# Performance work log

Measured on AMD Instinct MI355X. Metric: run time of the kernel, lower is better.

## Reference

```python
import jax, jax.numpy as jnp
import numpy as np

GRID = (32, 32)
LATENT = 256
ALPHA = 1.0
DECAY = 0.9


def _cdist(a, b):
    # Euclidean pairwise distance with a grad-safe sqrt (0 where d2==0, like torch.cdist).
    d2 = jnp.sum(a * a, -1)[:, None] + jnp.sum(b * b, -1)[None, :] - 2.0 * (a @ b.T)
    d2 = jnp.maximum(d2, 0.0)
    mask = d2 > 0
    return jnp.where(mask, jnp.sqrt(jnp.where(mask, d2, 1.0)), 0.0)


def setup_inputs() -> dict:
    key = jax.random.key(0)
    k1, k2 = jax.random.split(key)
    z = jax.random.normal(k1, (64, 512, 256), dtype=jnp.float32)
    nodes = jax.random.normal(k2, (GRID[0], GRID[1], LATENT), dtype=jnp.float32)
    return {"z": z, "nodes": nodes}


def reference(z, nodes):
    b, t, d = z.shape
    # time_decay^(seq_len - t - 1)
    tw = DECAY ** (t - 1 - jnp.arange(t, dtype=jnp.float32))
    z_flat = (z * tw[None, :, None]).reshape(b * t, d)   # (b t) d
    nodes_flat = nodes.reshape(-1, d)                     # n d

    dist = _cdist(z_flat, nodes_flat)                     # (b t) n
    q = 1.0 / (1.0 + dist / ALPHA) ** ((ALPHA + 1.0) / 2.0)
    q = q / jnp.sum(q, axis=-1, keepdims=True)            # L1 normalize rows
    q2 = q * q
    p = q2 / jnp.sum(q2, axis=0, keepdims=True)
    p = p / jnp.sum(p, axis=-1, keepdims=True)

    bmu = jnp.argmin(dist, axis=-1).reshape(b, t)         # int32

    # F.kl_div(q.log(), p, reduction='batchmean') = sum(p*(log p - log q)) / N
    kl_loss = jnp.sum(p * (jnp.log(p) - jnp.log(q))) / (b * t)
    diversity_loss = -jnp.mean(_cdist(nodes_flat, nodes_flat))
    time_smooth_loss = jnp.mean((z[:, 1:] - z[:, :-1]) ** 2) * DECAY

    # vectorized neighborhood consistency (python loop in the original is an
    # unweighted mean over all (b, t) adjacent pairs since seq_len is uniform)
    gw = GRID[1]
    pc = jnp.stack([bmu[:, :-1] // gw, bmu[:, :-1] % gw], axis=-1)
    nc = jnp.stack([bmu[:, 1:] // gw, bmu[:, 1:] % gw], axis=-1)
    neighbor_loss = jnp.mean(jnp.sum(jnp.abs(pc - nc), axis=-1).astype(jnp.float32))

    total_loss = kl_loss + 0.5 * diversity_loss + 0.3 * time_smooth_loss + 0.2 * neighbor_loss

    bmu_nodes = nodes_flat[bmu.reshape(-1)].reshape(b, t, d)
    som_z = z + 0.1 * (bmu_nodes - z)
    return (som_z, total_loss, kl_loss, diversity_loss, time_smooth_loss, neighbor_loss, q, bmu)
```

## Files before the change

kernel.cpp:

```cpp
#include <hip/hip_runtime.h>
#include <math.h>

#define Bb 64
#define Tt 512
#define Dd 256
#define Nn 1024
#define NROWS 32768

#define OUT_SOM 0L
#define OUT_SCAL 8388608L
#define OUT_Q 8388613L
#define OUT_BMU 41943045L

typedef __attribute__((ext_vector_type(8))) short bf16x8;
typedef __attribute__((ext_vector_type(4))) float f32x4;
typedef unsigned long long u64;

static __device__ __forceinline__ unsigned short f2bf(float x) {
  unsigned int u = __float_as_uint(x);
  unsigned int r = (u + 0x7fffu + ((u >> 16) & 1u)) >> 16;
  return (unsigned short)r;
}
static __device__ __forceinline__ float bf2f(unsigned short b) {
  return __uint_as_float(((unsigned int)b) << 16);
}

static __device__ __forceinline__ float block_reduce_sum(float v, float* sb) {
#pragma unroll
  for (int o = 32; o > 0; o >>= 1) v += __shfl_down(v, o, 64);
  const int lane = threadIdx.x & 63, w = threadIdx.x >> 6;
  if (lane == 0) sb[w] = v;
  __syncthreads();
  return (threadIdx.x == 0) ? (sb[0] + sb[1] + sb[2] + sb[3]) : 0.0f;
}

__global__ __launch_bounds__(256) void k_convz(const float* __restrict__ z,
                                               unsigned short* __restrict__ zhi,
                                               unsigned short* __restrict__ zlo,
                                               float* __restrict__ zn) {
  const int tid = threadIdx.x, lane = tid & 63, w = tid >> 6;
  const long row = (long)blockIdx.x * 4 + w;
  const int t = (int)(row & (Tt - 1));
  const float tw = powf(0.9f, (float)(Tt - 1 - t));
  const float4 v = ((const float4*)(z + row * Dd))[lane];
  float x[4] = {v.x * tw, v.y * tw, v.z * tw, v.w * tw};
  unsigned short h[4], l[4];
  float s = 0.f;
#pragma unroll
  for (int i = 0; i < 4; ++i) {
    h[i] = f2bf(x[i]);
    l[i] = f2bf(x[i] - bf2f(h[i]));
    s = fmaf(x[i], x[i], s);
  }
  *(ushort4*)(zhi + row * Dd + lane * 4) = make_ushort4(h[0], h[1], h[2], h[3]);
  *(ushort4*)(zlo + row * Dd + lane * 4) = make_ushort4(l[0], l[1], l[2], l[3]);
#pragma unroll
  for (int o = 32; o > 0; o >>= 1) s += __shfl_down(s, o, 64);
  if (lane == 0) zn[row] = s;
}

__global__ __launch_bounds__(256) void k_convn(const float* __restrict__ nodes,
                                               float* __restrict__ nt,
                                               float* __restrict__ nnorm,
                                               unsigned short* __restrict__ nhi,
                                               unsigned short* __restrict__ nlo) {
  __shared__ float sb[4];
  const int j = blockIdx.x, d = threadIdx.x;
  const float v = nodes[j * Dd + d];
  nt[(long)d * Nn + j] = v;
  const unsigned short h = f2bf(v);
  nhi[j * Dd + d] = h;
  nlo[j * Dd + d] = f2bf(v - bf2f(h));
  const float tot = block_reduce_sum(v * v, sb);
  if (threadIdx.x == 0) nnorm[j] = tot;
}

__global__ __launch_bounds__(256) void k_div(const float* __restrict__ nodes,
                                             const float* __restrict__ nt,
                                             const float* __restrict__ nnorm,
                                             float* __restrict__ scal) {
  __shared__ float ni[4][Dd];
  __shared__ float sb[4];
  const int tid = threadIdx.x;
  const int i0 = blockIdx.x * 4;
#pragma unroll
  for (int r = 0; r < 4; ++r) ni[r][tid] = nodes[(i0 + r) * Dd + tid];
  __syncthreads();
  float acc[4][4];
#pragma unroll
  for (int r = 0; r < 4; ++r)
#pragma unroll
    for (int jj = 0; jj < 4; ++jj) acc[r][jj] = 0.f;
  for (int d = 0; d < Dd; ++d) {
    float nj[4];
#pragma unroll
    for (int jj = 0; jj < 4; ++jj) nj[jj] = nt[(long)d * Nn + tid + 256 * jj];
#pragma unroll
    for (int r = 0; r < 4; ++r) {
      const float s = ni[r][d];
#pragma unroll
      for (int jj = 0; jj < 4; ++jj) acc[r][jj] = fmaf(s, nj[jj], acc[r][jj]);
    }
  }
  float sum = 0.f;
#pragma unroll
  for (int r = 0; r < 4; ++r) {
#pragma unroll
    for (int jj = 0; jj < 4; ++jj) {
      const float d2 = nnorm[i0 + r] + nnorm[tid + 256 * jj] - 2.f * acc[r][jj];
      sum += sqrtf(fmaxf(d2, 0.f));
    }
  }
  const float tot = block_reduce_sum(sum, sb);
  if (tid == 0) atomicAdd(&scal[1], tot);
}

__global__ __launch_bounds__(256, 2) void k_gemm(
    const unsigned short* __restrict__ zhi, const unsigned short* __restrict__ zlo,
    const unsigned short* __restrict__ nhi, const unsigned short* __restrict__ nlo,
    const float* __restrict__ zn, const float* __restrict__ nn,
    float* __restrict__ qout, float* __restrict__ part8,
    u64* __restrict__ bmup8) {
  __shared__ __align__(16) unsigned char smem[65536];

  const int tid = threadIdx.x, lane = tid & 63, wave = tid >> 6;
  const int wr = wave >> 1, wc = wave & 1;
  const int rl = lane & 15, kq = lane >> 4;
  const int bm = blockIdx.x & 255, bn = blockIdx.x >> 8;
  const long row0 = (long)bm * 128;
  const int col0 = bn * 128;

  auto stage = [&](int kt, int bufsel) {
    unsigned char* lb = smem + bufsel * 32768;
#pragma unroll
    for (int i = 0; i < 2; ++i) {
      const int rbase = (i * 4 + wave) * 16;
      const int r = rbase + (lane >> 2);
      const int kb = (lane & 3) ^ ((r >> 1) & 3);
      const long ea = (row0 + r) * Dd + kt * 32 + kb * 8;
      const long eb = (long)(col0 + r) * Dd + kt * 32 + kb * 8;
      const int lo = rbase * 64;
      __builtin_amdgcn_global_load_lds(
          (const __attribute__((address_space(1))) void*)(zhi + ea),
          (__attribute__((address_space(3))) void*)(lb + lo), 16, 0, 0);
      __builtin_amdgcn_global_load_lds(
          (const __attribute__((address_space(1))) void*)(zlo + ea),
          (__attribute__((address_space(3))) void*)(lb + 8192 + lo), 16, 0, 0);
      __builtin_amdgcn_global_load_lds(
          (const __attribute__((address_space(1))) void*)(nhi + eb),
          (__attribute__((address_space(3))) void*)(lb + 16384 + lo), 16, 0, 0);
      __builtin_amdgcn_global_load_lds(
          (const __attribute__((address_space(1))) void*)(nlo + eb),
          (__attribute__((address_space(3))) void*)(lb + 24576 + lo), 16, 0, 0);
    }
  };

  f32x4 acc[4][4];
#pragma unroll
  for (int i = 0; i < 4; ++i)
#pragma unroll
    for (int j = 0; j < 4; ++j) acc[i][j] = (f32x4){0.f, 0.f, 0.f, 0.f};

  stage(0, 0);
  __syncthreads();

  const int sx = (kq ^ ((rl >> 1) & 3)) << 4;

  for (int kt = 0; kt < 8; ++kt) {
    if (kt < 7) stage(kt + 1, (kt + 1) & 1);
    unsigned char* lb = smem + (kt & 1) * 32768;
    bf16x8 ah[4], al[4], bh[4], bl[4];
#pragma unroll
    for (int t = 0; t < 4; ++t) {
      const int ra = (wr * 64 + t * 16 + rl) * 64 + sx;
      ah[t] = *(const bf16x8*)(lb + ra);
      al[t] = *(const bf16x8*)(lb + 8192 + ra);
      const int rb = (wc * 64 + t * 16 + rl) * 64 + sx;
      bh[t] = *(const bf16x8*)(lb + 16384 + rb);
      bl[t] = *(const bf16x8*)(lb + 24576 + rb);
    }
#pragma unroll
    for (int i = 0; i < 4; ++i)
#pragma unroll
      for (int j = 0; j < 4; ++j) {
        acc[i][j] = __builtin_amdgcn_mfma_f32_16x16x32_bf16(ah[i], bh[j], acc[i][j], 0, 0, 0);
        acc[i][j] = __builtin_amdgcn_mfma_f32_16x16x32_bf16(ah[i], bl[j], acc[i][j], 0, 0, 0);
        acc[i][j] = __builtin_amdgcn_mfma_f32_16x16x32_bf16(al[i], bh[j], acc[i][j], 0, 0, 0);
      }
    __syncthreads();
  }

  float* srs = (float*)smem;
  u64* sbest = (u64*)(smem + 1024);
  float nnv[4];
#pragma unroll
  for (int j = 0; j < 4; ++j) nnv[j] = nn[col0 + wc * 64 + j * 16 + rl];

#pragma unroll
  for (int i = 0; i < 4; ++i) {
#pragma unroll
    for (int r = 0; r < 4; ++r) {
      const int lrow = wr * 64 + i * 16 + kq * 4 + r;
      const long grow = row0 + lrow;
      const float znv = zn[grow];
      float rs = 0.f;
      u64 best = ~0ull;
#pragma unroll
      for (int j = 0; j < 4; ++j) {
        const float dot = acc[i][j][r];
        const float d2 = znv + nnv[j] - 2.f * dot;
        const float dist = sqrtf(fmaxf(d2, 0.f));
        const float qr = 1.f / (1.f + dist);
        rs += qr;
        const int col = col0 + wc * 64 + j * 16 + rl;
        const u64 pk = ((u64)__float_as_uint(dist) << 32) | (unsigned int)col;
        best = pk < best ? pk : best;
        qout[grow * Nn + col] = qr;
      }
#pragma unroll
      for (int m = 1; m < 16; m <<= 1) {
        rs += __shfl_xor(rs, m, 64);
        const u64 o = __shfl_xor(best, m, 64);
        best = o < best ? o : best;
      }
      if (rl == 0) {
        srs[lrow * 2 + wc] = rs;
        sbest[lrow * 2 + wc] = best;
      }
    }
  }
  __syncthreads();
  if (tid < 128) {
    const long grow = row0 + tid;
    part8[grow * 8 + bn] = srs[tid * 2] + srs[tid * 2 + 1];
    const u64 a = sbest[tid * 2], b = sbest[tid * 2 + 1];
    bmup8[grow * 8 + bn] = a < b ? a : b;
  }
}

__global__ __launch_bounds__(256) void k_unpack(const u64* __restrict__ bmup8,
                                                float* __restrict__ bmuf) {
  const long row = (long)blockIdx.x * 256 + threadIdx.x;
  u64 best = ~0ull;
#pragma unroll
  for (int i = 0; i < 8; ++i) {
    const u64 v = bmup8[row * 8 + i];
    best = v < best ? v : best;
  }
  bmuf[row] = (float)(int)(unsigned int)(best & 0xffffffffull);
}

__global__ __launch_bounds__(256) void k_norm(float* __restrict__ q,
                                              const float* __restrict__ part8,
                                              float* __restrict__ colsum) {
  __shared__ float inv16[16];
  const int tid = threadIdx.x;
  const long r0 = (long)blockIdx.x * 16;
  if (tid < 16) {
    float s = 0.f;
    const float* p = part8 + (r0 + tid) * 8;
#pragma unroll
    for (int i = 0; i < 8; ++i) s += p[i];
    inv16[tid] = 1.f / s;
  }
  __syncthreads();
  float cs[4] = {0.f, 0.f, 0.f, 0.f};
  for (int r = 0; r < 16; ++r) {
    const long row = r0 + r;
    const float inv = inv16[r];
#pragma unroll
    for (int j = 0; j < 4; ++j) {
      const long idx = row * Nn + tid + 256 * j;
      const float v = q[idx] * inv;
      q[idx] = v;
      cs[j] = fmaf(v, v, cs[j]);
    }
  }
#pragma unroll
  for (int j = 0; j < 4; ++j) atomicAdd(&colsum[tid + 256 * j], cs[j]);
}

__global__ __launch_bounds__(256) void k_kl(const float* __restrict__ q,
                                            const float* __restrict__ colsum,
                                            float* __restrict__ scal) {
  __shared__ float csh[Nn];
  __shared__ float sb[4];
  const int tid = threadIdx.x, lane = tid & 63, wave = tid >> 6;
#pragma unroll
  for (int j = 0; j < 4; ++j) csh[tid + 256 * j] = colsum[tid + 256 * j];
  __syncthreads();
  const long r0 = (long)blockIdx.x * 16;
  float klp = 0.f;
  for (int rr = 0; rr < 4; ++rr) {
    const long row = r0 + rr * 4 + wave;
    float qv[16], u[16], s = 0.f;
#pragma unroll
    for (int j = 0; j < 16; ++j) {
      const int col = lane + 64 * j;
      const float t = q[row * Nn + col];
      qv[j] = t;
      const float uu = t * t / csh[col];
      u[j] = uu;
      s += uu;
    }
#pragma unroll
    for (int o = 1; o < 64; o <<= 1) s += __shfl_xor(s, o, 64);
    const float invS = 1.f / s;
#pragma unroll
    for (int j = 0; j < 16; ++j) {
      const float p = u[j] * invS;
      klp += p * (__logf(p) - __logf(qv[j]));
    }
  }
  const float tot = block_reduce_sum(klp, sb);
  if (tid == 0) atomicAdd(&scal[0], tot);
}

__global__ __launch_bounds__(256) void k_som(const float* __restrict__ z,
                                             const float* __restrict__ nodes,
                                             const float* __restrict__ bmuf,
                                             float* __restrict__ som,
                                             float* __restrict__ scal) {
  __shared__ float sb[4];
  const int tid = threadIdx.x;
  const long r0 = (long)blockIdx.x * 16;
  float ts = 0.f, zp = 0.f;
  if ((r0 & (Tt - 1)) > 0) zp = z[(r0 - 1) * Dd + tid];
  for (int r = 0; r < 16; ++r) {
    const long row = r0 + r;
    const float zc = z[row * Dd + tid];
    const int bi = (int)bmuf[row];
    const float nv = nodes[(long)bi * Dd + tid];
    som[row * Dd + tid] = zc + 0.1f * (nv - zc);
    if ((row & (Tt - 1)) > 0) {
      const float dd = zc - zp;
      ts = fmaf(dd, dd, ts);
    }
    zp = zc;
  }
  const float tot = block_reduce_sum(ts, sb);
  if (tid == 0) atomicAdd(&scal[2], tot);
}

__global__ __launch_bounds__(256) void k_nb(const float* __restrict__ bmuf,
                                            float* __restrict__ scal) {
  __shared__ float sb[4];
  const int idx = blockIdx.x * 256 + threadIdx.x;
  float s = 0.f;
  if (idx < Bb * (Tt - 1)) {
    const int b = idx / (Tt - 1);
    const int k = idx - b * (Tt - 1);
    const long row = (long)b * Tt + k;
    const int b1 = (int)bmuf[row], b2 = (int)bmuf[row + 1];
    s = (float)(abs((b1 >> 5) - (b2 >> 5)) + abs((b1 & 31) - (b2 & 31)));
  }
  const float tot = block_reduce_sum(s, sb);
  if (threadIdx.x == 0) atomicAdd(&scal[3], tot);
}

__global__ void k_final(const float* __restrict__ scal, float* __restrict__ o) {
  const float kl = scal[0] * (1.f / 32768.f);
  const float dv = -scal[1] * (1.f / (1024.f * 1024.f));
  const float ts = scal[2] * (0.9f / (64.f * 511.f * 256.f));
  const float nb = scal[3] * (1.f / 32704.f);
  o[0] = kl + 0.5f * dv + 0.3f * ts + 0.2f * nb;
  o[1] = kl;
  o[2] = dv;
  o[3] = ts;
  o[4] = nb;
}

__global__ __launch_bounds__(256) void k_prep_fb(const float* __restrict__ nodes,
                                                 float* __restrict__ nt,
                                                 float* __restrict__ nnorm) {
  __shared__ float sb[4];
  const int j = blockIdx.x, d = threadIdx.x;
  const float v = nodes[j * Dd + d];
  nt[(long)d * Nn + j] = v;
  const float tot = block_reduce_sum(v * v, sb);
  if (threadIdx.x == 0) nnorm[j] = tot;
}

__global__ __launch_bounds__(256) void k_dist_fb(
    const float* __restrict__ z, const float* __restrict__ nt,
    const float* __restrict__ nnorm, float* __restrict__ qout,
    float* __restrict__ srow, float* __restrict__ bmuf) {
  __shared__ float zt[Dd][65];
  __shared__ float rs4[4][64];
  __shared__ u64 cand[4][64];
  const int tid = threadIdx.x, lane = tid & 63, wave = tid >> 6;
  const long row0 = (long)blockIdx.x * 64;
  for (int k = 0; k < 64; ++k) {
    const int t = (int)((row0 + k) & (Tt - 1));
    const float tw = powf(0.9f, (float)(Tt - 1 - t));
    zt[tid][k] = z[(row0 + k) * Dd + tid] * tw;
  }
  __syncthreads();
  float zns = 0.f;
  for (int d = 0; d < Dd; ++d) {
    const float v = zt[d][lane];
    zns = fmaf(v, v, zns);
  }
  const long myrow = row0 + lane;
  float rsum = 0.f;
  u64 best = ~0ull;
  const int j0w = wave * 256;
  for (int chunk = 0; chunk < 16; ++chunk) {
    const int j0 = j0w + chunk * 16;
    float acc[16];
#pragma unroll
    for (int i = 0; i < 16; ++i) acc[i] = 0.f;
    const float* ntp = nt + j0;
    for (int d = 0; d < Dd; ++d) {
      const float zv = zt[d][lane];
      const float4 a = ((const float4*)ntp)[0];
      const float4 b = ((const float4*)ntp)[1];
      const float4 c = ((const float4*)ntp)[2];
      const float4 e = ((const float4*)ntp)[3];
      ntp += Nn;
      acc[0] = fmaf(zv, a.x, acc[0]); acc[1] = fmaf(zv, a.y, acc[1]);
      acc[2] = fmaf(zv, a.z, acc[2]); acc[3] = fmaf(zv, a.w, acc[3]);
      acc[4] = fmaf(zv, b.x, acc[4]); acc[5] = fmaf(zv, b.y, acc[5]);
      acc[6] = fmaf(zv, b.z, acc[6]); acc[7] = fmaf(zv, b.w, acc[7]);
      acc[8] = fmaf(zv, c.x, acc[8]); acc[9] = fmaf(zv, c.y, acc[9]);
      acc[10] = fmaf(zv, c.z, acc[10]); acc[11] = fmaf(zv, c.w, acc[11]);
      acc[12] = fmaf(zv, e.x, acc[12]); acc[13] = fmaf(zv, e.y, acc[13]);
      acc[14] = fmaf(zv, e.z, acc[14]); acc[15] = fmaf(zv, e.w, acc[15]);
    }
#pragma unroll
    for (int jj = 0; jj < 16; ++jj) {
      const int j = j0 + jj;
      const float d2 = zns + nnorm[j] - 2.f * acc[jj];
      const float dist = sqrtf(fmaxf(d2, 0.f));
      const float qr = 1.f / (1.f + dist);
      qout[myrow * Nn + j] = qr;
      rsum += qr;
      const u64 pk = ((u64)__float_as_uint(dist) << 32) | (unsigned int)j;
      best = pk < best ? pk : best;
    }
  }
  rs4[wave][lane] = rsum;
  cand[wave][lane] = best;
  __syncthreads();
  if (wave == 0) {
    const float s = rs4[0][lane] + rs4[1][lane] + rs4[2][lane] + rs4[3][lane];
    srow[myrow] = s;
    const u64 m0 = cand[0][lane] < cand[1][lane] ? cand[0][lane] : cand[1][lane];
    const u64 m1 = cand[2][lane] < cand[3][lane] ? cand[2][lane] : cand[3][lane];
    const u64 m = m0 < m1 ? m0 : m1;
    bmuf[myrow] = (float)(int)(unsigned int)(m & 0xffffffffull);
  }
}

__global__ __launch_bounds__(256) void k_norm_fb(float* __restrict__ q,
                                                 const float* __restrict__ srow,
                                                 float* __restrict__ colsum) {
  const int tid = threadIdx.x;
  const long r0 = (long)blockIdx.x * 16;
  float cs[4] = {0.f, 0.f, 0.f, 0.f};
  for (int r = 0; r < 16; ++r) {
    const long row = r0 + r;
    const float inv = 1.f / srow[row];
#pragma unroll
    for (int j = 0; j < 4; ++j) {
      const long idx = row * Nn + tid + 256 * j;
      const float v = q[idx] * inv;
      q[idx] = v;
      cs[j] = fmaf(v, v, cs[j]);
    }
  }
#pragma unroll
  for (int j = 0; j < 4; ++j) atomicAdd(&colsum[tid + 256 * j], cs[j]);
}

extern "C" void kernel_launch(void* const* d_in, const int* in_sizes, int n_in,
                              void* d_out, int out_size, void* d_ws, size_t ws_size,
                              hipStream_t stream) {
  const float* z = (const float*)d_in[0];
  const float* nodes = (const float*)d_in[1];
  float* out = (float*)d_out;
  unsigned char* ws = (unsigned char*)d_ws;

  float* som = out + OUT_SOM;
  float* scal_out = out + OUT_SCAL;
  float* qout = out + OUT_Q;
  float* bmuf = out + OUT_BMU;

  const size_t NEED = 37888016;
  if (ws_size >= NEED) {
    unsigned short* zhi = (unsigned short*)(ws + 0);
    unsigned short* zlo = (unsigned short*)(ws + 16777216);
    unsigned short* nhi = (unsigned short*)(ws + 33554432);
    unsigned short* nlo = (unsigned short*)(ws + 34078720);
    float* zn = (float*)(ws + 34603008);
    float* ntpart = (float*)(ws + 34734080);
    u64* bmup8 = (u64*)(ws + 35782656);
    float* nnorm = (float*)(ws + 37879808);
    float* colsum = (float*)(ws + 37883904);
    float* scal = (float*)(ws + 37888000);

    hipMemsetAsync(colsum, 0, 4096 + 16, stream);

    k_convz<<<8192, 256, 0, stream>>>(z, zhi, zlo, zn);
    k_convn<<<1024, 256, 0, stream>>>(nodes, ntpart, nnorm, nhi, nlo);
    k_div<<<256, 256, 0, stream>>>(nodes, ntpart, nnorm, scal);
    k_gemm<<<2048, 256, 0, stream>>>(zhi, zlo, nhi, nlo, zn, nnorm, qout, ntpart, bmup8);
    k_unpack<<<128, 256, 0, stream>>>(bmup8, bmuf);
    k_norm<<<2048, 256, 0, stream>>>(qout, ntpart, colsum);
    k_kl<<<2048, 256, 0, stream>>>(qout, colsum, scal);
    k_som<<<2048, 256, 0, stream>>>(z, nodes, bmuf, som, scal);
    k_nb<<<128, 256, 0, stream>>>(bmuf, scal);
    k_final<<<1, 1, 0, stream>>>(scal, scal_out);
  } else {
    float* wsf = (float*)ws;
    float* nt = wsf;
    float* nnorm = wsf + 262144;
    float* srow = wsf + 263168;
    float* colsum = wsf + 295936;
    float* scal = wsf + 296960;

    hipMemsetAsync(colsum, 0, (1024 + 4) * sizeof(float), stream);
    k_prep_fb<<<1024, 256, 0, stream>>>(nodes, nt, nnorm);
    k_div<<<256, 256, 0, stream>>>(nodes, nt, nnorm, scal);
    k_dist_fb<<<512, 256, 0, stream>>>(z, nt, nnorm, qout, srow, bmuf);
    k_norm_fb<<<2048, 256, 0, stream>>>(qout, srow, colsum);
    k_kl<<<2048, 256, 0, stream>>>(qout, colsum, scal);
    k_som<<<2048, 256, 0, stream>>>(z, nodes, bmuf, som, scal);
    k_nb<<<128, 256, 0, stream>>>(bmuf, scal);
    k_final<<<1, 1, 0, stream>>>(scal, scal_out);
  }
}
```

Measured before the change: 298.0 us.

## Fuse row normalization into GEMM, pre-swizzle MFMA operands, merge small kernels

The z and nodes conversion kernels are merged into one, and each writes bf16 hi/lo operands already arranged in MFMA fragment order. A new GEMM kernel processes 32 full rows per block across all 1024 columns, reading fragments straight from global memory without an LDS stage. Because whole rows stay in one block, it can finish the row-sum normalization, the BMU selection and the column-sum accumulation in place, which removes the separate unpack and normalize passes and their extra read/write of q. Other changes: the diversity loss moves to an MFMA kernel, the KL kernel is reworked algebraically to use one pass with precomputed reciprocal and log column sums, and the neighbor loss is folded into the som kernel. The cost is that GEMM operands are no longer reused through LDS, so global/L2 traffic for the node operands goes up.

```diff
diff --git a/kernel.cpp b/kernel.cpp
--- a/kernel.cpp
+++ b/kernel.cpp
@@ -15,6 +15,7 @@
 typedef __attribute__((ext_vector_type(8))) short bf16x8;
 typedef __attribute__((ext_vector_type(4))) float f32x4;
 typedef unsigned long long u64;
+typedef unsigned short ushortT;
 
 static __device__ __forceinline__ unsigned short f2bf(float x) {
   unsigned int u = __float_as_uint(x);
@@ -34,293 +35,312 @@
   return (threadIdx.x == 0) ? (sb[0] + sb[1] + sb[2] + sb[3]) : 0.0f;
 }
 
-__global__ __launch_bounds__(256) void k_convz(const float* __restrict__ z,
-                                               unsigned short* __restrict__ zhi,
-                                               unsigned short* __restrict__ zlo,
-                                               float* __restrict__ zn) {
+__global__ __launch_bounds__(256) void k_conv(
+    const float* __restrict__ z, const float* __restrict__ nodes,
+    ushortT* __restrict__ zhiF, ushortT* __restrict__ zloF, float* __restrict__ zn,
+    ushortT* __restrict__ nhiF, ushortT* __restrict__ nloF, float* __restrict__ nnorm) {
+  __shared__ float sm[32 * 260];
+  const int tid = threadIdx.x;
+  if (blockIdx.x < 1024) {
+    const int rt = blockIdx.x;
+    const long row0 = (long)rt * 32;
+    const int r = tid >> 3, c8 = tid & 7;
+    const long rowg = row0 + r;
+    const int t = (int)(rowg & (Tt - 1));
+    const float tw = powf(0.9f, (float)(Tt - 1 - t));
+    float nrm = 0.f;
+#pragma unroll
+    for (int k = 0; k < 8; ++k) {
+      const int c4 = c8 + k * 8;
+      float4 v = ((const float4*)(z + rowg * Dd))[c4];
+      v.x *= tw; v.y *= tw; v.z *= tw; v.w *= tw;
+      *(float4*)&sm[r * 260 + c4 * 4] = v;
+      nrm += v.x * v.x + v.y * v.y + v.z * v.z + v.w * v.w;
+    }
+    nrm += __shfl_xor(nrm, 1, 64);
+    nrm += __shfl_xor(nrm, 2, 64);
+    nrm += __shfl_xor(nrm, 4, 64);
+    if (c8 == 0) zn[rowg] = nrm;
+    __syncthreads();
+    ushort4* oh = (ushort4*)(zhiF + (long)rt * 8192);
+    ushort4* ol = (ushort4*)(zloF + (long)rt * 8192);
+#pragma unroll
+    for (int i = 0; i < 8; ++i) {
+      const int o4 = tid + 256 * i;
+      const int e4 = (o4 & 1) * 4;
+      const int r16 = (o4 >> 1) & 15;
+      const int k8 = (o4 >> 5) & 3;
+      const int g = (o4 >> 7) & 1;
+      const int ks = o4 >> 8;
+      const float* p = &sm[(g * 16 + r16) * 260 + ks * 32 + k8 * 8 + e4];
+      const float4 v = *(const float4*)p;
+      ushort4 h, l;
+      h.x = f2bf(v.x); l.x = f2bf(v.x - bf2f(h.x));
+      h.y = f2bf(v.y); l.y = f2bf(v.y - bf2f(h.y));
+      h.z = f2bf(v.z); l.z = f2bf(v.z - bf2f(h.z));
+      h.w = f2bf(v.w); l.w = f2bf(v.w - bf2f(h.w));
+      oh[o4] = h;
+      ol[o4] = l;
+    }
+  } else {
+    const int ct = blockIdx.x - 1024;
+    const int jr = tid >> 4, cg = tid & 15;
+    const long nrow = (long)(ct * 16 + jr);
+    float nrm = 0.f;
+#pragma unroll
+    for (int k = 0; k < 4; ++k) {
+      const int c4 = cg + k * 16;
+      const float4 v = ((const float4*)(nodes + nrow * Dd))[c4];
+      *(float4*)&sm[jr * 260 + c4 * 4] = v;
+      nrm += v.x * v.x + v.y * v.y + v.z * v.z + v.w * v.w;
+    }
+    nrm += __shfl_xor(nrm, 1, 64);
+    nrm += __shfl_xor(nrm, 2, 64);
+    nrm += __shfl_xor(nrm, 4, 64);
+    nrm += __shfl_xor(nrm, 8, 64);
+    if (cg == 0) nnorm[nrow] = nrm;
+    __syncthreads();
+    ushort4* oh = (ushort4*)(nhiF + (long)ct * 4096);
+    ushort4* ol = (ushort4*)(nloF + (long)ct * 4096);
+#pragma unroll
+    for (int i = 0; i < 4; ++i) {
+      const int o4 = tid + 256 * i;
+      const int e4 = (o4 & 1) * 4;
+      const int c16 = (o4 >> 1) & 15;
+      const int k8 = (o4 >> 5) & 3;
+      const int ks = o4 >> 7;
+      const float* p = &sm[c16 * 260 + ks * 32 + k8 * 8 + e4];
+      const float4 v = *(const float4*)p;
+      ushort4 h, l;
+      h.x = f2bf(v.x); l.x = f2bf(v.x - bf2f(h.x));
+      h.y = f2bf(v.y); l.y = f2bf(v.y - bf2f(h.y));
+      h.z = f2bf(v.z); l.z = f2bf(v.z - bf2f(h.z));
+      h.w = f2bf(v.w); l.w = f2bf(v.w - bf2f(h.w));
+      oh[o4] = h;
+      ol[o4] = l;
+    }
+  }
+}
+
+__global__ __launch_bounds__(512) void k_gemm2(
+    const ushortT* __restrict__ zhiF, const ushortT* __restrict__ zloF,
+    const ushortT* __restrict__ nhiF, const ushortT* __restrict__ nloF,
+    const float* __restrict__ zn, const float* __restrict__ nn,
+    float* __restrict__ qout, float* __restrict__ bmuf, float* __restrict__ colsum) {
+  __shared__ float srowS[32][8];
+  __shared__ u64 sbmu[32][8];
+  __shared__ float sinv[32];
   const int tid = threadIdx.x, lane = tid & 63, w = tid >> 6;
-  const long row = (long)blockIdx.x * 4 + w;
-  const int t = (int)(row & (Tt - 1));
-  const float tw = powf(0.9f, (float)(Tt - 1 - t));
-  const float4 v = ((const float4*)(z + row * Dd))[lane];
-  float x[4] = {v.x * tw, v.y * tw, v.z * tw, v.w * tw};
-  unsigned short h[4], l[4];
-  float s = 0.f;
-#pragma unroll
-  for (int i = 0; i < 4; ++i) {
-    h[i] = f2bf(x[i]);
-    l[i] = f2bf(x[i] - bf2f(h[i]));
-    s = fmaf(x[i], x[i], s);
-  }
-  *(ushort4*)(zhi + row * Dd + lane * 4) = make_ushort4(h[0], h[1], h[2], h[3]);
-  *(ushort4*)(zlo + row * Dd + lane * 4) = make_ushort4(l[0], l[1], l[2], l[3]);
-#pragma unroll
-  for (int o = 32; o > 0; o >>= 1) s += __shfl_down(s, o, 64);
-  if (lane == 0) zn[row] = s;
-}
-
-__global__ __launch_bounds__(256) void k_convn(const float* __restrict__ nodes,
-                                               float* __restrict__ nt,
-                                               float* __restrict__ nnorm,
-                                               unsigned short* __restrict__ nhi,
-                                               unsigned short* __restrict__ nlo) {
-  __shared__ float sb[4];
-  const int j = blockIdx.x, d = threadIdx.x;
-  const float v = nodes[j * Dd + d];
-  nt[(long)d * Nn + j] = v;
-  const unsigned short h = f2bf(v);
-  nhi[j * Dd + d] = h;
-  nlo[j * Dd + d] = f2bf(v - bf2f(h));
-  const float tot = block_reduce_sum(v * v, sb);
-  if (threadIdx.x == 0) nnorm[j] = tot;
-}
-
-__global__ __launch_bounds__(256) void k_div(const float* __restrict__ nodes,
-                                             const float* __restrict__ nt,
-                                             const float* __restrict__ nnorm,
-                                             float* __restrict__ scal) {
-  __shared__ float ni[4][Dd];
-  __shared__ float sb[4];
-  const int tid = threadIdx.x;
-  const int i0 = blockIdx.x * 4;
-#pragma unroll
-  for (int r = 0; r < 4; ++r) ni[r][tid] = nodes[(i0 + r) * Dd + tid];
-  __syncthreads();
-  float acc[4][4];
-#pragma unroll
-  for (int r = 0; r < 4; ++r)
-#pragma unroll
-    for (int jj = 0; jj < 4; ++jj) acc[r][jj] = 0.f;
-  for (int d = 0; d < Dd; ++d) {
-    float nj[4];
-#pragma unroll
-    for (int jj = 0; jj < 4; ++jj) nj[jj] = nt[(long)d * Nn + tid + 256 * jj];
+  const int rl = lane & 15, kq = lane >> 4;
+  const int rt = blockIdx.x;
+  const long row0 = (long)rt * 32;
+
+  const ushortT* Ah = zhiF + (long)rt * 8192;
+  const ushortT* Al = zloF + (long)rt * 8192;
+  const ushortT* Bh = nhiF + (long)w * 8 * 4096;
+  const ushortT* Bl = nloF + (long)w * 8 * 4096;
+  const int lo8 = lane * 8;
+
+  f32x4 acc[2][8];
+#pragma unroll
+  for (int g = 0; g < 2; ++g)
+#pragma unroll
+    for (int c = 0; c < 8; ++c) acc[g][c] = (f32x4){0.f, 0.f, 0.f, 0.f};
+
+#pragma unroll 1
+  for (int ks = 0; ks < 8; ++ks) {
+    const bf16x8 ah0 = *(const bf16x8*)(Ah + (ks * 2 + 0) * 512 + lo8);
+    const bf16x8 ah1 = *(const bf16x8*)(Ah + (ks * 2 + 1) * 512 + lo8);
+    const bf16x8 al0 = *(const bf16x8*)(Al + (ks * 2 + 0) * 512 + lo8);
+    const bf16x8 al1 = *(const bf16x8*)(Al + (ks * 2 + 1) * 512 + lo8);
+#pragma unroll
+    for (int c = 0; c < 8; ++c) {
+      const bf16x8 bh = *(const bf16x8*)(Bh + c * 4096 + ks * 512 + lo8);
+      const bf16x8 bl = *(const bf16x8*)(Bl + c * 4096 + ks * 512 + lo8);
+      acc[0][c] = __builtin_amdgcn_mfma_f32_16x16x32_bf16(ah0, bh, acc[0][c], 0, 0, 0);
+      acc[0][c] = __builtin_amdgcn_mfma_f32_16x16x32_bf16(ah0, bl, acc[0][c], 0, 0, 0);
+      acc[0][c] = __builtin_amdgcn_mfma_f32_16x16x32_bf16(al0, bh, acc[0][c], 0, 0, 0);
+      acc[1][c] = __builtin_amdgcn_mfma_f32_16x16x32_bf16(ah1, bh, acc[1][c], 0, 0, 0);
+      acc[1][c] = __builtin_amdgcn_mfma_f32_16x16x32_bf16(ah1, bl, acc[1][c], 0, 0, 0);
+      acc[1][c] = __builtin_amdgcn_mfma_f32_16x16x32_bf16(al1, bh, acc[1][c], 0, 0, 0);
+    }
+  }
+
+  float znv[2][4], nnv[8];
+#pragma unroll
+  for (int g = 0; g < 2; ++g)
+#pragma unroll
+    for (int r = 0; r < 4; ++r) znv[g][r] = zn[row0 + g * 16 + kq * 4 + r];
+#pragma unroll
+  for (int c = 0; c < 8; ++c) nnv[c] = nn[w * 128 + c * 16 + rl];
+
+  float rs[2][4];
+  u64 bm[2][4];
+#pragma unroll
+  for (int g = 0; g < 2; ++g)
+#pragma unroll
+    for (int r = 0; r < 4; ++r) { rs[g][r] = 0.f; bm[g][r] = ~0ull; }
+
+#pragma unroll
+  for (int g = 0; g < 2; ++g)
+#pragma unroll
+    for (int c = 0; c < 8; ++c)
+#pragma unroll
+      for (int r = 0; r < 4; ++r) {
+        const float dot = acc[g][c][r];
+        const float d2 = znv[g][r] + nnv[c] - 2.f * dot;
+        const float dist = sqrtf(fmaxf(d2, 0.f));
+        const float qv = 1.f / (1.f + dist);
+        acc[g][c][r] = qv;
+        rs[g][r] += qv;
+        const int col = w * 128 + c * 16 + rl;
+        const u64 pk = ((u64)__float_as_uint(dist) << 32) | (unsigned int)col;
+        bm[g][r] = pk < bm[g][r] ? pk : bm[g][r];
+      }
+#pragma unroll
+  for (int g = 0; g < 2; ++g)
 #pragma unroll
     for (int r = 0; r < 4; ++r) {
-      const float s = ni[r][d];
-#pragma unroll
-      for (int jj = 0; jj < 4; ++jj) acc[r][jj] = fmaf(s, nj[jj], acc[r][jj]);
-    }
-  }
-  float sum = 0.f;
-#pragma unroll
-  for (int r = 0; r < 4; ++r) {
-#pragma unroll
-    for (int jj = 0; jj < 4; ++jj) {
-      const float d2 = nnorm[i0 + r] + nnorm[tid + 256 * jj] - 2.f * acc[r][jj];
-      sum += sqrtf(fmaxf(d2, 0.f));
-    }
-  }
-  const float tot = block_reduce_sum(sum, sb);
-  if (tid == 0) atomicAdd(&scal[1], tot);
-}
-
-__global__ __launch_bounds__(256, 2) void k_gemm(
-    const unsigned short* __restrict__ zhi, const unsigned short* __restrict__ zlo,
-    const unsigned short* __restrict__ nhi, const unsigned short* __restrict__ nlo,
-    const float* __restrict__ zn, const float* __restrict__ nn,
-    float* __restrict__ qout, float* __restrict__ part8,
-    u64* __restrict__ bmup8) {
-  __shared__ __align__(16) unsigned char smem[65536];
-
-  const int tid = threadIdx.x, lane = tid & 63, wave = tid >> 6;
-  const int wr = wave >> 1, wc = wave & 1;
-  const int rl = lane & 15, kq = lane >> 4;
-  const int bm = blockIdx.x & 255, bn = blockIdx.x >> 8;
-  const long row0 = (long)bm * 128;
-  const int col0 = bn * 128;
-
-  auto stage = [&](int kt, int bufsel) {
-    unsigned char* lb = smem + bufsel * 32768;
-#pragma unroll
-    for (int i = 0; i < 2; ++i) {
-      const int rbase = (i * 4 + wave) * 16;
-      const int r = rbase + (lane >> 2);
-      const int kb = (lane & 3) ^ ((r >> 1) & 3);
-      const long ea = (row0 + r) * Dd + kt * 32 + kb * 8;
-      const long eb = (long)(col0 + r) * Dd + kt * 32 + kb * 8;
-      const int lo = rbase * 64;
-      __builtin_amdgcn_global_load_lds(
-          (const __attribute__((address_space(1))) void*)(zhi + ea),
-          (__attribute__((address_space(3))) void*)(lb + lo), 16, 0, 0);
-      __builtin_amdgcn_global_load_lds(
-          (const __attribute__((address_space(1))) void*)(zlo + ea),
-          (__attribute__((address_space(3))) void*)(lb + 8192 + lo), 16, 0, 0);
-      __builtin_amdgcn_global_load_lds(
-          (const __attribute__((address_space(1))) void*)(nhi + eb),
-          (__attribute__((address_space(3))) void*)(lb + 16384 + lo), 16, 0, 0);
-      __builtin_amdgcn_global_load_lds(
-          (const __attribute__((address_space(1))) void*)(nlo + eb),
-          (__attribute__((address_space(3))) void*)(lb + 24576 + lo), 16, 0, 0);
-    }
-  };
-
-  f32x4 acc[4][4];
-#pragma unroll
-  for (int i = 0; i < 4; ++i)
-#pragma unroll
-    for (int j = 0; j < 4; ++j) acc[i][j] = (f32x4){0.f, 0.f, 0.f, 0.f};
-
-  stage(0, 0);
-  __syncthreads();
-
-  const int sx = (kq ^ ((rl >> 1) & 3)) << 4;
-
-  for (int kt = 0; kt < 8; ++kt) {
-    if (kt < 7) stage(kt + 1, (kt + 1) & 1);
-    unsigned char* lb = smem + (kt & 1) * 32768;
-    bf16x8 ah[4], al[4], bh[4], bl[4];
-#pragma unroll
-    for (int t = 0; t < 4; ++t) {
-      const int ra = (wr * 64 + t * 16 + rl) * 64 + sx;
-      ah[t] = *(const bf16x8*)(lb + ra);
-      al[t] = *(const bf16x8*)(lb + 8192 + ra);
-      const int rb = (wc * 64 + t * 16 + rl) * 64 + sx;
-      bh[t] = *(const bf16x8*)(lb + 16384 + rb);
-      bl[t] = *(const bf16x8*)(lb + 24576 + rb);
-    }
-#pragma unroll
-    for (int i = 0; i < 4; ++i)
-#pragma unroll
-      for (int j = 0; j < 4; ++j) {
-        acc[i][j] = __builtin_amdgcn_mfma_f32_16x16x32_bf16(ah[i], bh[j], acc[i][j], 0, 0, 0);
-        acc[i][j] = __builtin_amdgcn_mfma_f32_16x16x32_bf16(ah[i], bl[j], acc[i][j], 0, 0, 0);
-        acc[i][j] = __builtin_amdgcn_mfma_f32_16x16x32_bf16(al[i], bh[j], acc[i][j], 0, 0, 0);
-      }
-    __syncthreads();
-  }
-
-  float* srs = (float*)smem;
-  u64* sbest = (u64*)(smem + 1024);
-  float nnv[4];
-#pragma unroll
-  for (int j = 0; j < 4; ++j) nnv[j] = nn[col0 + wc * 64 + j * 16 + rl];
-
-#pragma unroll
-  for (int i = 0; i < 4; ++i) {
-#pragma unroll
-    for (int r = 0; r < 4; ++r) {
-      const int lrow = wr * 64 + i * 16 + kq * 4 + r;
-      const long grow = row0 + lrow;
-      const float znv = zn[grow];
-      float rs = 0.f;
-      u64 best = ~0ull;
-#pragma unroll
-      for (int j = 0; j < 4; ++j) {
-        const float dot = acc[i][j][r];
-        const float d2 = znv + nnv[j] - 2.f * dot;
-        const float dist = sqrtf(fmaxf(d2, 0.f));
-        const float qr = 1.f / (1.f + dist);
-        rs += qr;
-        const int col = col0 + wc * 64 + j * 16 + rl;
-        const u64 pk = ((u64)__float_as_uint(dist) << 32) | (unsigned int)col;
-        best = pk < best ? pk : best;
-        qout[grow * Nn + col] = qr;
-      }
 #pragma unroll
       for (int m = 1; m < 16; m <<= 1) {
-        rs += __shfl_xor(rs, m, 64);
-        const u64 o = __shfl_xor(best, m, 64);
-        best = o < best ? o : best;
+        rs[g][r] += __shfl_xor(rs[g][r], m, 64);
+        const u64 o = __shfl_xor(bm[g][r], m, 64);
+        bm[g][r] = o < bm[g][r] ? o : bm[g][r];
       }
       if (rl == 0) {
-        srs[lrow * 2 + wc] = rs;
-        sbest[lrow * 2 + wc] = best;
+        srowS[g * 16 + kq * 4 + r][w] = rs[g][r];
+        sbmu[g * 16 + kq * 4 + r][w] = bm[g][r];
       }
     }
-  }
-  __syncthreads();
-  if (tid < 128) {
-    const long grow = row0 + tid;
-    part8[grow * 8 + bn] = srs[tid * 2] + srs[tid * 2 + 1];
-    const u64 a = sbest[tid * 2], b = sbest[tid * 2 + 1];
-    bmup8[grow * 8 + bn] = a < b ? a : b;
-  }
-}
-
-__global__ __launch_bounds__(256) void k_unpack(const u64* __restrict__ bmup8,
-                                                float* __restrict__ bmuf) {
-  const long row = (long)blockIdx.x * 256 + threadIdx.x;
-  u64 best = ~0ull;
-#pragma unroll
-  for (int i = 0; i < 8; ++i) {
-    const u64 v = bmup8[row * 8 + i];
-    best = v < best ? v : best;
-  }
-  bmuf[row] = (float)(int)(unsigned int)(best & 0xffffffffull);
-}
-
-__global__ __launch_bounds__(256) void k_norm(float* __restrict__ q,
-                                              const float* __restrict__ part8,
-                                              float* __restrict__ colsum) {
-  __shared__ float inv16[16];
-  const int tid = threadIdx.x;
-  const long r0 = (long)blockIdx.x * 16;
-  if (tid < 16) {
+  __syncthreads();
+  if (tid < 32) {
     float s = 0.f;
-    const float* p = part8 + (r0 + tid) * 8;
-#pragma unroll
-    for (int i = 0; i < 8; ++i) s += p[i];
-    inv16[tid] = 1.f / s;
-  }
-  __syncthreads();
-  float cs[4] = {0.f, 0.f, 0.f, 0.f};
-  for (int r = 0; r < 16; ++r) {
-    const long row = r0 + r;
-    const float inv = inv16[r];
-#pragma unroll
-    for (int j = 0; j < 4; ++j) {
-      const long idx = row * Nn + tid + 256 * j;
-      const float v = q[idx] * inv;
-      q[idx] = v;
-      cs[j] = fmaf(v, v, cs[j]);
-    }
-  }
-#pragma unroll
-  for (int j = 0; j < 4; ++j) atomicAdd(&colsum[tid + 256 * j], cs[j]);
+    u64 best = ~0ull;
+#pragma unroll
+    for (int i = 0; i < 8; ++i) {
+      s += srowS[tid][i];
+      const u64 v = sbmu[tid][i];
+      best = v < best ? v : best;
+    }
+    sinv[tid] = 1.f / s;
+    bmuf[row0 + tid] = (float)(int)(unsigned int)(best & 0xffffffffull);
+  }
+  __syncthreads();
+
+  float inv[2][4];
+#pragma unroll
+  for (int g = 0; g < 2; ++g)
+#pragma unroll
+    for (int r = 0; r < 4; ++r) inv[g][r] = sinv[g * 16 + kq * 4 + r];
+
+  float cp[8];
+#pragma unroll
+  for (int c = 0; c < 8; ++c) cp[c] = 0.f;
+#pragma unroll
+  for (int g = 0; g < 2; ++g)
+#pragma unroll
+    for (int c = 0; c < 8; ++c)
+#pragma unroll
+      for (int r = 0; r < 4; ++r) {
+        const float qn = acc[g][c][r] * inv[g][r];
+        qout[(row0 + g * 16 + kq * 4 + r) * Nn + w * 128 + c * 16 + rl] = qn;
+        cp[c] = fmaf(qn, qn, cp[c]);
+      }
+#pragma unroll
+  for (int c = 0; c < 8; ++c) {
+    cp[c] += __shfl_xor(cp[c], 16, 64);
+    cp[c] += __shfl_xor(cp[c], 32, 64);
+    if (kq == 0) atomicAdd(&colsum[w * 128 + c * 16 + rl], cp[c]);
+  }
+}
+
+__global__ __launch_bounds__(256) void k_div2(
+    const ushortT* __restrict__ nhiF, const ushortT* __restrict__ nloF,
+    const float* __restrict__ nnorm, float* __restrict__ scal) {
+  __shared__ float sb[4];
+  const int tid = threadIdx.x, lane = tid & 63, w = tid >> 6;
+  const int rl = lane & 15, kq = lane >> 4;
+  const int bi = blockIdx.x;
+  const int lo8 = lane * 8;
+
+  f32x4 acc[16];
+#pragma unroll
+  for (int c = 0; c < 16; ++c) acc[c] = (f32x4){0.f, 0.f, 0.f, 0.f};
+
+#pragma unroll 1
+  for (int ks = 0; ks < 8; ++ks) {
+    const bf16x8 ah = *(const bf16x8*)(nhiF + (long)bi * 4096 + ks * 512 + lo8);
+    const bf16x8 al = *(const bf16x8*)(nloF + (long)bi * 4096 + ks * 512 + lo8);
+#pragma unroll
+    for (int c = 0; c < 16; ++c) {
+      const long ct = (long)(w * 16 + c);
+      const bf16x8 bh = *(const bf16x8*)(nhiF + ct * 4096 + ks * 512 + lo8);
+      const bf16x8 bl = *(const bf16x8*)(nloF + ct * 4096 + ks * 512 + lo8);
+      acc[c] = __builtin_amdgcn_mfma_f32_16x16x32_bf16(ah, bh, acc[c], 0, 0, 0);
+      acc[c] = __builtin_amdgcn_mfma_f32_16x16x32_bf16(ah, bl, acc[c], 0, 0, 0);
+      acc[c] = __builtin_amdgcn_mfma_f32_16x16x32_bf16(al, bh, acc[c], 0, 0, 0);
+    }
+  }
+  float ni[4];
+#pragma unroll
+  for (int r = 0; r < 4; ++r) ni[r] = nnorm[bi * 16 + kq * 4 + r];
+  float dsum = 0.f;
+#pragma unroll
+  for (int c = 0; c < 16; ++c) {
+    const float nj = nnorm[w * 256 + c * 16 + rl];
+#pragma unroll
+    for (int r = 0; r < 4; ++r) {
+      const float d2 = ni[r] + nj - 2.f * acc[c][r];
+      dsum += sqrtf(fmaxf(d2, 0.f));
+    }
+  }
+  const float tot = block_reduce_sum(dsum, sb);
+  if (tid == 0) atomicAdd(&scal[1], tot);
 }
 
 __global__ __launch_bounds__(256) void k_kl(const float* __restrict__ q,
                                             const float* __restrict__ colsum,
                                             float* __restrict__ scal) {
-  __shared__ float csh[Nn];
+  __shared__ float rcs[Nn];
+  __shared__ float lcs[Nn];
   __shared__ float sb[4];
   const int tid = threadIdx.x, lane = tid & 63, wave = tid >> 6;
 #pragma unroll
-  for (int j = 0; j < 4; ++j) csh[tid + 256 * j] = colsum[tid + 256 * j];
+  for (int j = 0; j < 4; ++j) {
+    const float cs = colsum[tid + 256 * j];
+    rcs[tid + 256 * j] = 1.f / cs;
+    lcs[tid + 256 * j] = __logf(cs);
+  }
   __syncthreads();
   const long r0 = (long)blockIdx.x * 16;
   float klp = 0.f;
   for (int rr = 0; rr < 4; ++rr) {
     const long row = r0 + rr * 4 + wave;
-    float qv[16], u[16], s = 0.f;
+    float s = 0.f, a = 0.f;
 #pragma unroll
     for (int j = 0; j < 16; ++j) {
       const int col = lane + 64 * j;
       const float t = q[row * Nn + col];
-      qv[j] = t;
-      const float uu = t * t / csh[col];
-      u[j] = uu;
-      s += uu;
-    }
-#pragma unroll
-    for (int o = 1; o < 64; o <<= 1) s += __shfl_xor(s, o, 64);
-    const float invS = 1.f / s;
-#pragma unroll
-    for (int j = 0; j < 16; ++j) {
-      const float p = u[j] * invS;
-      klp += p * (__logf(p) - __logf(qv[j]));
-    }
+      const float u = t * t * rcs[col];
+      s += u;
+      a = fmaf(u, __logf(t) - lcs[col], a);
+    }
+#pragma unroll
+    for (int o = 1; o < 64; o <<= 1) {
+      s += __shfl_xor(s, o, 64);
+      a += __shfl_xor(a, o, 64);
+    }
+    if (lane == 0) klp += a / s - __logf(s);
   }
   const float tot = block_reduce_sum(klp, sb);
   if (tid == 0) atomicAdd(&scal[0], tot);
 }
 
-__global__ __launch_bounds__(256) void k_som(const float* __restrict__ z,
-                                             const float* __restrict__ nodes,
-                                             const float* __restrict__ bmuf,
-                                             float* __restrict__ som,
-                                             float* __restrict__ scal) {
+__global__ __launch_bounds__(256) void k_somnb(const float* __restrict__ z,
+                                               const float* __restrict__ nodes,
+                                               const float* __restrict__ bmuf,
+                                               float* __restrict__ som,
+                                               float* __restrict__ scal) {
   __shared__ float sb[4];
   const int tid = threadIdx.x;
   const long r0 = (long)blockIdx.x * 16;
@@ -338,24 +358,19 @@
     }
     zp = zc;
   }
-  const float tot = block_reduce_sum(ts, sb);
-  if (tid == 0) atomicAdd(&scal[2], tot);
-}
-
-__global__ __launch_bounds__(256) void k_nb(const float* __restrict__ bmuf,
-                                            float* __restrict__ scal) {
-  __shared__ float sb[4];
-  const int idx = blockIdx.x * 256 + threadIdx.x;
-  float s = 0.f;
-  if (idx < Bb * (Tt - 1)) {
-    const int b = idx / (Tt - 1);
-    const int k = idx - b * (Tt - 1);
-    const long row = (long)b * Tt + k;
-    const int b1 = (int)bmuf[row], b2 = (int)bmuf[row + 1];
-    s = (float)(abs((b1 >> 5) - (b2 >> 5)) + abs((b1 & 31) - (b2 & 31)));
-  }
-  const float tot = block_reduce_sum(s, sb);
-  if (threadIdx.x == 0) atomicAdd(&scal[3], tot);
+  const float tts = block_reduce_sum(ts, sb);
+  if (tid == 0) atomicAdd(&scal[2], tts);
+  float nbv = 0.f;
+  if (tid < 16) {
+    const long row = r0 + tid;
+    if ((row & (Tt - 1)) != (Tt - 1)) {
+      const int b1 = (int)bmuf[row], b2 = (int)bmuf[row + 1];
+      nbv = (float)(abs((b1 >> 5) - (b2 >> 5)) + abs((b1 & 31) - (b2 & 31)));
+    }
+  }
+  __syncthreads();
+  const float tnb = block_reduce_sum(nbv, sb);
+  if (tid == 0) atomicAdd(&scal[3], tnb);
 }
 
 __global__ void k_final(const float* __restrict__ scal, float* __restrict__ o) {
@@ -379,6 +394,45 @@
   nt[(long)d * Nn + j] = v;
   const float tot = block_reduce_sum(v * v, sb);
   if (threadIdx.x == 0) nnorm[j] = tot;
+}
+
+__global__ __launch_bounds__(256) void k_div_fb(const float* __restrict__ nodes,
+                                                const float* __restrict__ nt,
+                                                const float* __restrict__ nnorm,
+                                                float* __restrict__ scal) {
+  __shared__ float ni[4][Dd];
+  __shared__ float sb[4];
+  const int tid = threadIdx.x;
+  const int i0 = blockIdx.x * 4;
+#pragma unroll
+  for (int r = 0; r < 4; ++r) ni[r][tid] = nodes[(i0 + r) * Dd + tid];
+  __syncthreads();
+  float acc[4][4];
+#pragma unroll
+  for (int r = 0; r < 4; ++r)
+#pragma unroll
+    for (int jj = 0; jj < 4; ++jj) acc[r][jj] = 0.f;
+  for (int d = 0; d < Dd; ++d) {
+    float nj[4];
+#pragma unroll
+    for (int jj = 0; jj < 4; ++jj) nj[jj] = nt[(long)d * Nn + tid + 256 * jj];
+#pragma unroll
+    for (int r = 0; r < 4; ++r) {
+      const float s = ni[r][d];
+#pragma unroll
+      for (int jj = 0; jj < 4; ++jj) acc[r][jj] = fmaf(s, nj[jj], acc[r][jj]);
+    }
+  }
+  float sum = 0.f;
+#pragma unroll
+  for (int r = 0; r < 4; ++r)
+#pragma unroll
+    for (int jj = 0; jj < 4; ++jj) {
+      const float d2 = nnorm[i0 + r] + nnorm[tid + 256 * jj] - 2.f * acc[r][jj];
+      sum += sqrtf(fmaxf(d2, 0.f));
+    }
+  const float tot = block_reduce_sum(sum, sb);
+  if (tid == 0) atomicAdd(&scal[1], tot);
 }
 
 __global__ __launch_bounds__(256) void k_dist_fb(
@@ -486,30 +540,24 @@
   float* qout = out + OUT_Q;
   float* bmuf = out + OUT_BMU;
 
-  const size_t NEED = 37888016;
+  const size_t NEED = 34742288;
   if (ws_size >= NEED) {
-    unsigned short* zhi = (unsigned short*)(ws + 0);
-    unsigned short* zlo = (unsigned short*)(ws + 16777216);
-    unsigned short* nhi = (unsigned short*)(ws + 33554432);
-    unsigned short* nlo = (unsigned short*)(ws + 34078720);
+    ushortT* zhiF = (ushortT*)(ws + 0);
+    ushortT* zloF = (ushortT*)(ws + 16777216);
+    ushortT* nhiF = (ushortT*)(ws + 33554432);
+    ushortT* nloF = (ushortT*)(ws + 34078720);
     float* zn = (float*)(ws + 34603008);
-    float* ntpart = (float*)(ws + 34734080);
-    u64* bmup8 = (u64*)(ws + 35782656);
-    float* nnorm = (float*)(ws + 37879808);
-    float* colsum = (float*)(ws + 37883904);
-    float* scal = (float*)(ws + 37888000);
+    float* nnorm = (float*)(ws + 34734080);
+    float* colsum = (float*)(ws + 34738176);
+    float* scal = (float*)(ws + 34742272);
 
     hipMemsetAsync(colsum, 0, 4096 + 16, stream);
 
-    k_convz<<<8192, 256, 0, stream>>>(z, zhi, zlo, zn);
-    k_convn<<<1024, 256, 0, stream>>>(nodes, ntpart, nnorm, nhi, nlo);
-    k_div<<<256, 256, 0, stream>>>(nodes, ntpart, nnorm, scal);
-    k_gemm<<<2048, 256, 0, stream>>>(zhi, zlo, nhi, nlo, zn, nnorm, qout, ntpart, bmup8);
-    k_unpack<<<128, 256, 0, stream>>>(bmup8, bmuf);
-    k_norm<<<2048, 256, 0, stream>>>(qout, ntpart, colsum);
+    k_conv<<<1088, 256, 0, stream>>>(z, nodes, zhiF, zloF, zn, nhiF, nloF, nnorm);
+    k_gemm2<<<1024, 512, 0, stream>>>(zhiF, zloF, nhiF, nloF, zn, nnorm, qout, bmuf, colsum);
+    k_div2<<<64, 256, 0, stream>>>(nhiF, nloF, nnorm, scal);
     k_kl<<<2048, 256, 0, stream>>>(qout, colsum, scal);
-    k_som<<<2048, 256, 0, stream>>>(z, nodes, bmuf, som, scal);
-    k_nb<<<128, 256, 0, stream>>>(bmuf, scal);
+    k_somnb<<<2048, 256, 0, stream>>>(z, nodes, bmuf, som, scal);
     k_final<<<1, 1, 0, stream>>>(scal, scal_out);
   } else {
     float* wsf = (float*)ws;
@@ -521,12 +569,11 @@
 
     hipMemsetAsync(colsum, 0, (1024 + 4) * sizeof(float), stream);
     k_prep_fb<<<1024, 256, 0, stream>>>(nodes, nt, nnorm);
-    k_div<<<256, 256, 0, stream>>>(nodes, nt, nnorm, scal);
+    k_div_fb<<<256, 256, 0, stream>>>(nodes, nt, nnorm, scal);
     k_dist_fb<<<512, 256, 0, stream>>>(z, nt, nnorm, qout, srow, bmuf);
     k_norm_fb<<<2048, 256, 0, stream>>>(qout, srow, colsum);
     k_kl<<<2048, 256, 0, stream>>>(qout, colsum, scal);
-    k_som<<<2048, 256, 0, stream>>>(z, nodes, bmuf, som, scal);
-    k_nb<<<128, 256, 0, stream>>>(bmuf, scal);
+    k_somnb<<<2048, 256, 0, stream>>>(z, nodes, bmuf, som, scal);
     k_final<<<1, 1, 0, stream>>>(scal, scal_out);
   }
 }
```

Measured after the change: 277.5 us. 6.9% less time.
